# Performance work log

Measured on AMD Instinct MI355X. Metric: run time of the kernel, lower is better.

The kernel has to match this reference:

```python
import jax, jax.numpy as jnp
import numpy as np

D_EMBED = 1024
D_HEAD = 128


def setup_inputs() -> dict:
    key = jax.random.key(0)
    kx, kq, kk, kv = jax.random.split(key, 4)
    x = jax.random.normal(kx, (4, 4096, D_EMBED), dtype=jnp.float32)
    # nn.Linear(d_embed, d_head, bias=False) weights, stored [out, in] like torch
    s = 1.0 / np.sqrt(D_EMBED)
    Wq = jax.random.uniform(kq, (D_HEAD, D_EMBED), jnp.float32, -s, s)
    Wk = jax.random.uniform(kk, (D_HEAD, D_EMBED), jnp.float32, -s, s)
    Wv = jax.random.uniform(kv, (D_HEAD, D_EMBED), jnp.float32, -s, s)
    return {"x": x, "Wq": Wq, "Wk": Wk, "Wv": Wv}


def reference(x, Wq, Wk, Wv):
    # q,k,v: [b, s, d_head]
    q = jnp.einsum("bse,he->bsh", x, Wq)
    k = jnp.einsum("bse,he->bsh", x, Wk)
    v = jnp.einsum("bse,he->bsh", x, Wv)
    # original: (q @ k^T) * d_head**-0.5, then divided by sqrt(d_embed)
    scale = 1.0 / (np.sqrt(D_HEAD) * np.sqrt(D_EMBED))
    scores = jnp.einsum("bqh,bkh->bqk", q, k) * jnp.float32(scale)  # [b, s, s]
    attn = jax.nn.softmax(scores, axis=-1)
    return jnp.einsum("bqk,bkh->bqh", attn, v)
```

## Files before the change

### kernel.cpp

```cpp
#include <hip/hip_runtime.h>
#include <stdint.h>

typedef __bf16 bf16x8 __attribute__((ext_vector_type(8)));
typedef float  f32x4  __attribute__((ext_vector_type(4)));

#define ATTN_SCALE 2.7621359e-3f

__device__ __forceinline__ unsigned short f2bf(float f) {
  union { float f; uint32_t u; } v; v.f = f;
  uint32_t u = v.u;
  uint32_t r = (u + 0x7FFFu + ((u >> 16) & 1u)) >> 16;
  return (unsigned short)r;
}

__device__ __forceinline__ void load_lds16(const unsigned short* g, unsigned short* l) {
  __builtin_amdgcn_global_load_lds(
      (const __attribute__((address_space(1))) void*)g,
      (__attribute__((address_space(3))) void*)l, 16, 0, 0);
}

__device__ __forceinline__ f32x4 mfma16(bf16x8 a, bf16x8 b, f32x4 c) {
  return __builtin_amdgcn_mfma_f32_16x16x32_bf16(a, b, c, 0, 0, 0);
}

__device__ __forceinline__ bf16x8 ones_bf16() {
  union { unsigned short u[8]; bf16x8 v; } c;
#pragma unroll
  for (int j = 0; j < 8; ++j) c.u[j] = 0x3F80;
  return c.v;
}

__global__ __launch_bounds__(256) void k_cvtw(const float* __restrict__ a,
                                              const float* __restrict__ b,
                                              const float* __restrict__ c,
                                              unsigned short* __restrict__ dst) {
  int i = blockIdx.x * 256 + threadIdx.x;
  int sel = i >> 15, off = i & 32767;
  const float* s = (sel == 0) ? a : (sel == 1) ? b : c;
  float4 f = ((const float4*)s)[off];
  ushort4 o;
  o.x = f2bf(f.x); o.y = f2bf(f.y); o.z = f2bf(f.z); o.w = f2bf(f.w);
  ((ushort4*)dst)[i] = o;
}

__global__ __launch_bounds__(256, 3) void k_proj(
    const float* __restrict__ X,
    const unsigned short* __restrict__ W,
    unsigned short* __restrict__ Qb,
    unsigned short* __restrict__ Kb,
    unsigned short* __restrict__ Vt)
{
  __shared__ __align__(16) unsigned short sm[2048 + 4096];
  unsigned short* As = sm;
  unsigned short* Bs = sm + 2048;
  const int t = threadIdx.x;
  const int mtile = blockIdx.x;
  const int nt = blockIdx.y;
  const int w = t >> 6, lane = t & 63, quad = lane >> 4, l15 = lane & 15;
  const int wm = w & 1, wn = w >> 1;

  const float* ag0 = X + (size_t)(mtile * 64 + (t >> 2)) * 1024 + (t & 3) * 8;
  const unsigned short* bg0 = W + (size_t)nt * 131072 + (size_t)(t >> 2) * 1024 + (t & 3) * 8;
  unsigned short* aw = &As[(t >> 2) * 32 + (t & 3) * 8];
  unsigned short* bw = &Bs[(t >> 2) * 32 + (t & 3) * 8];

  f32x4 acc[2][4] = {};

  for (int kt = 0; kt < 32; ++kt) {
    float4 a0 = *(const float4*)(ag0 + kt * 32);
    float4 a1 = *(const float4*)(ag0 + kt * 32 + 4);
    __syncthreads();
    load_lds16(bg0 + kt * 32,             bw);
    load_lds16(bg0 + kt * 32 + 64 * 1024, bw + 2048);
    union { unsigned short u[8]; uint4 v; } pa;
    pa.u[0] = f2bf(a0.x); pa.u[1] = f2bf(a0.y);
    pa.u[2] = f2bf(a0.z); pa.u[3] = f2bf(a0.w);
    pa.u[4] = f2bf(a1.x); pa.u[5] = f2bf(a1.y);
    pa.u[6] = f2bf(a1.z); pa.u[7] = f2bf(a1.w);
    *(uint4*)aw = pa.v;
    __syncthreads();

    bf16x8 af[2], bfr[4];
#pragma unroll
    for (int i = 0; i < 2; ++i)
      af[i] = *(const bf16x8*)&As[(wm * 32 + i * 16 + l15) * 32 + quad * 8];
#pragma unroll
    for (int j = 0; j < 4; ++j)
      bfr[j] = *(const bf16x8*)&Bs[(wn * 64 + j * 16 + l15) * 32 + quad * 8];
#pragma unroll
    for (int i = 0; i < 2; ++i)
#pragma unroll
      for (int j = 0; j < 4; ++j)
        acc[i][j] = mfma16(af[i], bfr[j], acc[i][j]);
  }

  if (nt != 2) {
    const int m0 = mtile * 64 + wm * 32;
#pragma unroll
    for (int i = 0; i < 2; ++i)
#pragma unroll
      for (int j = 0; j < 4; ++j)
#pragma unroll
        for (int r = 0; r < 4; ++r) {
          int m = m0 + i * 16 + quad * 4 + r;
          int n = wn * 64 + j * 16 + l15;
          float v = acc[i][j][r];
          if (nt == 0) Qb[(size_t)m * 128 + n] = f2bf(v * ATTN_SCALE);
          else         Kb[(size_t)m * 128 + n] = f2bf(v);
        }
  } else {
    float* Ts = (float*)sm;
    const int bb = mtile >> 6;
    const int s0 = (mtile & 63) * 64;
#pragma unroll
    for (int jj = 0; jj < 8; ++jj) {
      __syncthreads();
      if (wn == (jj >> 2)) {
        const int j = jj & 3;
#pragma unroll
        for (int i = 0; i < 2; ++i)
#pragma unroll
          for (int r = 0; r < 4; ++r)
            Ts[(wm * 32 + i * 16 + quad * 4 + r) * 17 + l15] = acc[i][j][r];
      }
      __syncthreads();
      int n2 = jj * 16 + (t >> 4);
      int m2 = (t & 15) * 4;
      union { unsigned short u[4]; uint2 v; } pk;
#pragma unroll
      for (int e = 0; e < 4; ++e) pk.u[e] = f2bf(Ts[(m2 + e) * 17 + (t >> 4)]);
      *(uint2*)&Vt[((size_t)(bb * 128 + n2)) * 4096 + s0 + m2] = pk.v;
    }
  }
}

__global__ __launch_bounds__(256, 3) void k_flash(
    const unsigned short* __restrict__ Qb,
    const unsigned short* __restrict__ Kb,
    const unsigned short* __restrict__ Vt,
    float* __restrict__ Om,
    float* __restrict__ lp)
{
  __shared__ __align__(16) unsigned short smem[21504];
  unsigned short* Psh = smem + 16384;
  float* Ob  = (float*)smem;
  float* lsh = (float*)(smem + 16384);

  const int t = threadIdx.x;
  const int w = t >> 6, lane = t & 63, quad = lane >> 4, l15 = lane & 15;
  const int h = w & 1, p = w >> 1;
  const int bid = blockIdx.x;
  const int b   = (bid & 7) >> 1;
  const int sp  = bid & 1;
  const int qt  = bid >> 3;

  const unsigned short* Qg = Qb + (size_t)(b * 4096 + qt * 64 + h * 32) * 128;
  const unsigned short* Kg = Kb + (size_t)b * 4096 * 128;
  const unsigned short* Vg = Vt + (size_t)b * 128 * 4096;

  bf16x8 qf[2][4];
#pragma unroll
  for (int mt = 0; mt < 2; ++mt)
#pragma unroll
    for (int kk = 0; kk < 4; ++kk)
      qf[mt][kk] = *(const bf16x8*)&Qg[(size_t)(mt * 16 + l15) * 128 + kk * 32 + quad * 8];

  f32x4 O[2][8] = {};
  f32x4 Ol[2] = {};

  const unsigned short* kg0 = Kg + (size_t)(t >> 4) * 128 + (((t & 15) ^ ((t >> 5) & 7)) * 8);
  const unsigned short* vg0 = Vg + (size_t)(t >> 3) * 4096 + (((t & 7) ^ ((t >> 3) & 7)) * 8);
  unsigned short* kw = &smem[w * 512];
  unsigned short* vw = &smem[8192 + w * 512];

  const int kt0 = sp * 32;

  {
    const unsigned short* kg = kg0 + (size_t)kt0 * 8192;
#pragma unroll
    for (int it = 0; it < 4; ++it)
      load_lds16(kg + it * 2048, kw + it * 2048);
  }

  for (int i = 0; i < 32; ++i) {
    const int kt = kt0 + i;
    const int ktn = (i < 31) ? (kt + 1) : kt0;

    asm volatile("s_waitcnt vmcnt(0)" ::: "memory");
    asm volatile("s_barrier" ::: "memory");

    {
      const unsigned short* vg = vg0 + (size_t)kt * 64;
#pragma unroll
      for (int it = 0; it < 4; ++it)
        load_lds16(vg + (size_t)it * 131072, vw + it * 2048);
    }

    f32x4 sc[2][2] = {};
#pragma unroll
    for (int ntk = 0; ntk < 2; ++ntk) {
      const int row = p * 32 + 2 * l15 + ntk;
#pragma unroll
      for (int kk = 0; kk < 4; ++kk) {
        bf16x8 kf = *(const bf16x8*)&smem[row * 128 + (((kk * 4 + quad) ^ (l15 & 7)) * 8)];
        sc[0][ntk] = mfma16(qf[0][kk], kf, sc[0][ntk]);
        sc[1][ntk] = mfma16(qf[1][kk], kf, sc[1][ntk]);
      }
    }

#pragma unroll
    for (int mt = 0; mt < 2; ++mt)
#pragma unroll
      for (int r = 0; r < 4; ++r) {
        float e0 = __expf(sc[mt][0][r]);
        float e1 = __expf(sc[mt][1][r]);
        int row = mt * 16 + quad * 4 + r;
        uint32_t pk = (uint32_t)f2bf(e0) | ((uint32_t)f2bf(e1) << 16);
        *(uint32_t*)&Psh[w * 1280 + row * 40 + 2 * l15] = pk;
      }

    asm volatile("s_waitcnt vmcnt(0) lgkmcnt(0)" ::: "memory");
    asm volatile("s_barrier" ::: "memory");

    {
      const unsigned short* kg = kg0 + (size_t)ktn * 8192;
#pragma unroll
      for (int it = 0; it < 4; ++it)
        load_lds16(kg + it * 2048, kw + it * 2048);
    }

    bf16x8 pf0 = *(const bf16x8*)&Psh[w * 1280 + l15 * 40 + quad * 8];
    bf16x8 pf1 = *(const bf16x8*)&Psh[w * 1280 + (16 + l15) * 40 + quad * 8];
    const bf16x8 one = ones_bf16();
    Ol[0] = mfma16(pf0, one, Ol[0]);
    Ol[1] = mfma16(pf1, one, Ol[1]);
    const unsigned short* Vshc = &smem[8192];
#pragma unroll
    for (int dt = 0; dt < 8; ++dt) {
      bf16x8 vf = *(const bf16x8*)&Vshc[(dt * 16 + l15) * 64 + (((p * 4 + quad) ^ (l15 & 7)) * 8)];
      O[0][dt] = mfma16(pf0, vf, O[0][dt]);
      O[1][dt] = mfma16(pf1, vf, O[1][dt]);
    }
  }

  __syncthreads();
  if (p == 1) {
#pragma unroll
    for (int mt = 0; mt < 2; ++mt)
#pragma unroll
      for (int r = 0; r < 4; ++r) {
        int row = h * 32 + mt * 16 + quad * 4 + r;
        if (l15 == 0) lsh[row] = Ol[mt][r];
#pragma unroll
        for (int dt = 0; dt < 8; ++dt)
          Ob[row * 128 + dt * 16 + l15] = O[mt][dt][r];
      }
  }
  __syncthreads();
  if (p == 0) {
    const size_t rowbase = (size_t)b * 4096 + qt * 64;
    float* Omp = Om + (size_t)sp * 2097152;
#pragma unroll
    for (int mt = 0; mt < 2; ++mt)
#pragma unroll
      for (int r = 0; r < 4; ++r) {
        int row = h * 32 + mt * 16 + quad * 4 + r;
#pragma unroll
        for (int dt = 0; dt < 8; ++dt)
          Omp[(rowbase + row) * 128 + dt * 16 + l15] =
              O[mt][dt][r] + Ob[row * 128 + dt * 16 + l15];
        if (l15 == 0)
          lp[(size_t)sp * 16384 + rowbase + row] = Ol[mt][r] + lsh[row];
      }
  }
}

__global__ __launch_bounds__(256) void k_merge(const float* __restrict__ Om,
                                               const float* __restrict__ lp,
                                               float* __restrict__ out) {
  int i = blockIdx.x * 256 + threadIdx.x;
  int row = i >> 5;
  float inv = 1.0f / (lp[row] + lp[16384 + row]);
  float4 a = ((const float4*)Om)[i];
  float4 c = ((const float4*)Om)[524288 + i];
  float4 o;
  o.x = (a.x + c.x) * inv;
  o.y = (a.y + c.y) * inv;
  o.z = (a.z + c.z) * inv;
  o.w = (a.w + c.w) * inv;
  ((float4*)out)[i] = o;
}

extern "C" void kernel_launch(void* const* d_in, const int* in_sizes, int n_in,
                              void* d_out, int out_size, void* d_ws, size_t ws_size,
                              hipStream_t stream) {
  const float* x  = (const float*)d_in[0];
  const float* Wq = (const float*)d_in[1];
  const float* Wk = (const float*)d_in[2];
  const float* Wv = (const float*)d_in[3];
  float* out = (float*)d_out;

  unsigned short* ws  = (unsigned short*)d_ws;
  unsigned short* wbf = ws;
  unsigned short* Qb  = wbf + 393216;
  unsigned short* Kb  = Qb + 2097152;
  unsigned short* Vt  = Kb + 2097152;
  float* Om = (float*)(Vt + 2097152);
  float* lp = Om + 4194304;

  k_cvtw<<<384, 256, 0, stream>>>(Wq, Wk, Wv, wbf);
  k_proj<<<dim3(256, 3), 256, 0, stream>>>(x, wbf, Qb, Kb, Vt);
  k_flash<<<512, 256, 0, stream>>>(Qb, Kb, Vt, Om, lp);
  k_merge<<<2048, 256, 0, stream>>>(Om, lp, out);
}
```

Baseline: 178.5 us.

## Fuse QKV projection into one block per row tile; stagger flash K/V order

The projection kernel now computes Q, K and V together in one block per 64-row tile, each warp covering 96 output columns. X is read and converted to bf16 once instead of three times, and the next X tile is prefetched into registers. The grid drops from 768 to 256 blocks with occupancy 1, which risks lower parallelism and more register pressure. The flash kernel also rotates the starting KV tile per query tile so concurrent blocks read different K/V rows, easing cache and channel contention.

```diff
diff --git a/kernel.cpp b/kernel.cpp
--- a/kernel.cpp
+++ b/kernel.cpp
@@ -43,94 +43,101 @@
   ((ushort4*)dst)[i] = o;
 }
 
-__global__ __launch_bounds__(256, 3) void k_proj(
+__global__ __launch_bounds__(256, 1) void k_proj(
     const float* __restrict__ X,
     const unsigned short* __restrict__ W,
     unsigned short* __restrict__ Qb,
     unsigned short* __restrict__ Kb,
     unsigned short* __restrict__ Vt)
 {
-  __shared__ __align__(16) unsigned short sm[2048 + 4096];
+  __shared__ __align__(16) unsigned short sm[2048 + 12288];
   unsigned short* As = sm;
   unsigned short* Bs = sm + 2048;
   const int t = threadIdx.x;
   const int mtile = blockIdx.x;
-  const int nt = blockIdx.y;
   const int w = t >> 6, lane = t & 63, quad = lane >> 4, l15 = lane & 15;
-  const int wm = w & 1, wn = w >> 1;
 
   const float* ag0 = X + (size_t)(mtile * 64 + (t >> 2)) * 1024 + (t & 3) * 8;
-  const unsigned short* bg0 = W + (size_t)nt * 131072 + (size_t)(t >> 2) * 1024 + (t & 3) * 8;
-  unsigned short* aw = &As[(t >> 2) * 32 + (t & 3) * 8];
-  unsigned short* bw = &Bs[(t >> 2) * 32 + (t & 3) * 8];
-
-  f32x4 acc[2][4] = {};
+  const unsigned short* bg0 = W + (size_t)(t >> 2) * 1024 + (t & 3) * 8;
+  unsigned short* aw = &As[t * 8];
+  unsigned short* bw = &Bs[t * 8];
+
+  f32x4 acc[4][6] = {};
+
+  float4 a0 = *(const float4*)(ag0);
+  float4 a1 = *(const float4*)(ag0 + 4);
 
   for (int kt = 0; kt < 32; ++kt) {
-    float4 a0 = *(const float4*)(ag0 + kt * 32);
-    float4 a1 = *(const float4*)(ag0 + kt * 32 + 4);
     __syncthreads();
-    load_lds16(bg0 + kt * 32,             bw);
-    load_lds16(bg0 + kt * 32 + 64 * 1024, bw + 2048);
+#pragma unroll
+    for (int it = 0; it < 6; ++it)
+      load_lds16(bg0 + kt * 32 + it * 65536, bw + it * 2048);
     union { unsigned short u[8]; uint4 v; } pa;
     pa.u[0] = f2bf(a0.x); pa.u[1] = f2bf(a0.y);
     pa.u[2] = f2bf(a0.z); pa.u[3] = f2bf(a0.w);
     pa.u[4] = f2bf(a1.x); pa.u[5] = f2bf(a1.y);
     pa.u[6] = f2bf(a1.z); pa.u[7] = f2bf(a1.w);
     *(uint4*)aw = pa.v;
+    if (kt < 31) {
+      a0 = *(const float4*)(ag0 + (kt + 1) * 32);
+      a1 = *(const float4*)(ag0 + (kt + 1) * 32 + 4);
+    }
     __syncthreads();
 
-    bf16x8 af[2], bfr[4];
-#pragma unroll
-    for (int i = 0; i < 2; ++i)
-      af[i] = *(const bf16x8*)&As[(wm * 32 + i * 16 + l15) * 32 + quad * 8];
-#pragma unroll
-    for (int j = 0; j < 4; ++j)
-      bfr[j] = *(const bf16x8*)&Bs[(wn * 64 + j * 16 + l15) * 32 + quad * 8];
-#pragma unroll
-    for (int i = 0; i < 2; ++i)
-#pragma unroll
-      for (int j = 0; j < 4; ++j)
+    bf16x8 af[4], bfr[6];
+#pragma unroll
+    for (int i = 0; i < 4; ++i)
+      af[i] = *(const bf16x8*)&As[(i * 16 + l15) * 32 + quad * 8];
+#pragma unroll
+    for (int j = 0; j < 6; ++j)
+      bfr[j] = *(const bf16x8*)&Bs[(w * 96 + j * 16 + l15) * 32 + quad * 8];
+#pragma unroll
+    for (int i = 0; i < 4; ++i)
+#pragma unroll
+      for (int j = 0; j < 6; ++j)
         acc[i][j] = mfma16(af[i], bfr[j], acc[i][j]);
   }
 
-  if (nt != 2) {
-    const int m0 = mtile * 64 + wm * 32;
-#pragma unroll
-    for (int i = 0; i < 2; ++i)
-#pragma unroll
-      for (int j = 0; j < 4; ++j)
+  const int m0 = mtile * 64;
+#pragma unroll
+  for (int j = 0; j < 6; ++j) {
+    const int f = w * 6 + j;
+    if (f < 16) {
+#pragma unroll
+      for (int i = 0; i < 4; ++i)
 #pragma unroll
         for (int r = 0; r < 4; ++r) {
           int m = m0 + i * 16 + quad * 4 + r;
-          int n = wn * 64 + j * 16 + l15;
+          int n = f * 16 + l15;
           float v = acc[i][j][r];
-          if (nt == 0) Qb[(size_t)m * 128 + n] = f2bf(v * ATTN_SCALE);
-          else         Kb[(size_t)m * 128 + n] = f2bf(v);
+          if (f < 8) Qb[(size_t)m * 128 + n]         = f2bf(v * ATTN_SCALE);
+          else       Kb[(size_t)m * 128 + (n - 128)] = f2bf(v);
         }
-  } else {
-    float* Ts = (float*)sm;
-    const int bb = mtile >> 6;
-    const int s0 = (mtile & 63) * 64;
-#pragma unroll
-    for (int jj = 0; jj < 8; ++jj) {
-      __syncthreads();
-      if (wn == (jj >> 2)) {
-        const int j = jj & 3;
-#pragma unroll
-        for (int i = 0; i < 2; ++i)
-#pragma unroll
-          for (int r = 0; r < 4; ++r)
-            Ts[(wm * 32 + i * 16 + quad * 4 + r) * 17 + l15] = acc[i][j][r];
-      }
-      __syncthreads();
-      int n2 = jj * 16 + (t >> 4);
-      int m2 = (t & 15) * 4;
-      union { unsigned short u[4]; uint2 v; } pk;
-#pragma unroll
-      for (int e = 0; e < 4; ++e) pk.u[e] = f2bf(Ts[(m2 + e) * 17 + (t >> 4)]);
-      *(uint2*)&Vt[((size_t)(bb * 128 + n2)) * 4096 + s0 + m2] = pk.v;
-    }
+    }
+  }
+
+  float* Ts = (float*)sm;
+  const int bb = mtile >> 6;
+  const int s0 = (mtile & 63) * 64;
+#pragma unroll
+  for (int c = 0; c < 8; ++c) {
+    const int wv = (c < 2) ? 2 : 3;
+    const int jv = (c < 2) ? (4 + c) : (c - 2);
+    __syncthreads();
+    if (w == wv) {
+#pragma unroll
+      for (int i = 0; i < 4; ++i)
+#pragma unroll
+        for (int r = 0; r < 4; ++r)
+          Ts[(i * 16 + quad * 4 + r) * 17 + l15] = acc[i][jv][r];
+    }
+    __syncthreads();
+    int n2 = c * 16 + (t >> 4);
+    int m2 = (t & 15) * 4;
+    union { unsigned short u[4]; uint2 v; } pk;
+#pragma unroll
+    for (int e = 0; e < 4; ++e) pk.u[e] = f2bf(Ts[(m2 + e) * 17 + (t >> 4)]);
+    *(uint2*)&Vt[((size_t)(bb * 128 + n2)) * 4096 + s0 + m2] = pk.v;
   }
 }
 
@@ -174,17 +181,18 @@
   unsigned short* vw = &smem[8192 + w * 512];
 
   const int kt0 = sp * 32;
+  const int off = (qt & 3) * 8;
 
   {
-    const unsigned short* kg = kg0 + (size_t)kt0 * 8192;
+    const unsigned short* kg = kg0 + (size_t)(kt0 + off) * 8192;
 #pragma unroll
     for (int it = 0; it < 4; ++it)
       load_lds16(kg + it * 2048, kw + it * 2048);
   }
 
   for (int i = 0; i < 32; ++i) {
-    const int kt = kt0 + i;
-    const int ktn = (i < 31) ? (kt + 1) : kt0;
+    const int kt  = kt0 + ((i + off) & 31);
+    const int ktn = kt0 + ((i + 1 + off) & 31);
 
     asm volatile("s_waitcnt vmcnt(0)" ::: "memory");
     asm volatile("s_barrier" ::: "memory");
@@ -309,7 +317,7 @@
   float* lp = Om + 4194304;
 
   k_cvtw<<<384, 256, 0, stream>>>(Wq, Wk, Wv, wbf);
-  k_proj<<<dim3(256, 3), 256, 0, stream>>>(x, wbf, Qb, Kb, Vt);
+  k_proj<<<256, 256, 0, stream>>>(x, wbf, Qb, Kb, Vt);
   k_flash<<<512, 256, 0, stream>>>(Qb, Kb, Vt, Om, lp);
   k_merge<<<2048, 256, 0, stream>>>(Om, lp, out);
 }
```

After: 193.0 us. 8.1% more time.

## Fuse weight bf16 conversion into projection kernel and prefetch next K tile

Applied to the files above, without the earlier changes.

Drops the separate weight-conversion kernel launch. The projection kernel now reads fp32 weights directly, converts them to bf16 in registers and writes them to LDS. It also register-prefetches the next k-tile of X and W while the current tile is being computed. This removes one launch and the intermediate weight buffer round-trip. In exchange each projection block redundantly converts weights, reads twice the weight bytes, and uses more registers.

```diff
diff --git a/kernel.cpp b/kernel.cpp
--- a/kernel.cpp
+++ b/kernel.cpp
@@ -30,22 +30,11 @@
   return c.v;
 }
 
-__global__ __launch_bounds__(256) void k_cvtw(const float* __restrict__ a,
-                                              const float* __restrict__ b,
-                                              const float* __restrict__ c,
-                                              unsigned short* __restrict__ dst) {
-  int i = blockIdx.x * 256 + threadIdx.x;
-  int sel = i >> 15, off = i & 32767;
-  const float* s = (sel == 0) ? a : (sel == 1) ? b : c;
-  float4 f = ((const float4*)s)[off];
-  ushort4 o;
-  o.x = f2bf(f.x); o.y = f2bf(f.y); o.z = f2bf(f.z); o.w = f2bf(f.w);
-  ((ushort4*)dst)[i] = o;
-}
-
 __global__ __launch_bounds__(256, 3) void k_proj(
     const float* __restrict__ X,
-    const unsigned short* __restrict__ W,
+    const float* __restrict__ Wq,
+    const float* __restrict__ Wk,
+    const float* __restrict__ Wv,
     unsigned short* __restrict__ Qb,
     unsigned short* __restrict__ Kb,
     unsigned short* __restrict__ Vt)
@@ -59,25 +48,51 @@
   const int w = t >> 6, lane = t & 63, quad = lane >> 4, l15 = lane & 15;
   const int wm = w & 1, wn = w >> 1;
 
+  const float* Wsel = (nt == 0) ? Wq : (nt == 1) ? Wk : Wv;
+
   const float* ag0 = X + (size_t)(mtile * 64 + (t >> 2)) * 1024 + (t & 3) * 8;
-  const unsigned short* bg0 = W + (size_t)nt * 131072 + (size_t)(t >> 2) * 1024 + (t & 3) * 8;
-  unsigned short* aw = &As[(t >> 2) * 32 + (t & 3) * 8];
-  unsigned short* bw = &Bs[(t >> 2) * 32 + (t & 3) * 8];
+  const float* bg0 = Wsel + (size_t)(t >> 2) * 1024 + (t & 3) * 8;
+  unsigned short* aw = &As[t * 8];
+  unsigned short* bw = &Bs[t * 8];
 
   f32x4 acc[2][4] = {};
 
+  float4 a0 = *(const float4*)(ag0);
+  float4 a1 = *(const float4*)(ag0 + 4);
+  float4 b0 = *(const float4*)(bg0);
+  float4 b1 = *(const float4*)(bg0 + 4);
+  float4 b2 = *(const float4*)(bg0 + 65536);
+  float4 b3 = *(const float4*)(bg0 + 65536 + 4);
+
   for (int kt = 0; kt < 32; ++kt) {
-    float4 a0 = *(const float4*)(ag0 + kt * 32);
-    float4 a1 = *(const float4*)(ag0 + kt * 32 + 4);
     __syncthreads();
-    load_lds16(bg0 + kt * 32,             bw);
-    load_lds16(bg0 + kt * 32 + 64 * 1024, bw + 2048);
-    union { unsigned short u[8]; uint4 v; } pa;
-    pa.u[0] = f2bf(a0.x); pa.u[1] = f2bf(a0.y);
-    pa.u[2] = f2bf(a0.z); pa.u[3] = f2bf(a0.w);
-    pa.u[4] = f2bf(a1.x); pa.u[5] = f2bf(a1.y);
-    pa.u[6] = f2bf(a1.z); pa.u[7] = f2bf(a1.w);
-    *(uint4*)aw = pa.v;
+    {
+      union { unsigned short u[8]; uint4 v; } pa;
+      pa.u[0] = f2bf(a0.x); pa.u[1] = f2bf(a0.y);
+      pa.u[2] = f2bf(a0.z); pa.u[3] = f2bf(a0.w);
+      pa.u[4] = f2bf(a1.x); pa.u[5] = f2bf(a1.y);
+      pa.u[6] = f2bf(a1.z); pa.u[7] = f2bf(a1.w);
+      *(uint4*)aw = pa.v;
+      union { unsigned short u[8]; uint4 v; } pb;
+      pb.u[0] = f2bf(b0.x); pb.u[1] = f2bf(b0.y);
+      pb.u[2] = f2bf(b0.z); pb.u[3] = f2bf(b0.w);
+      pb.u[4] = f2bf(b1.x); pb.u[5] = f2bf(b1.y);
+      pb.u[6] = f2bf(b1.z); pb.u[7] = f2bf(b1.w);
+      *(uint4*)bw = pb.v;
+      pb.u[0] = f2bf(b2.x); pb.u[1] = f2bf(b2.y);
+      pb.u[2] = f2bf(b2.z); pb.u[3] = f2bf(b2.w);
+      pb.u[4] = f2bf(b3.x); pb.u[5] = f2bf(b3.y);
+      pb.u[6] = f2bf(b3.z); pb.u[7] = f2bf(b3.w);
+      *(uint4*)(bw + 2048) = pb.v;
+    }
+    if (kt < 31) {
+      a0 = *(const float4*)(ag0 + (kt + 1) * 32);
+      a1 = *(const float4*)(ag0 + (kt + 1) * 32 + 4);
+      b0 = *(const float4*)(bg0 + (kt + 1) * 32);
+      b1 = *(const float4*)(bg0 + (kt + 1) * 32 + 4);
+      b2 = *(const float4*)(bg0 + (kt + 1) * 32 + 65536);
+      b3 = *(const float4*)(bg0 + (kt + 1) * 32 + 65536 + 4);
+    }
     __syncthreads();
 
     bf16x8 af[2], bfr[4];
@@ -301,15 +316,13 @@
   float* out = (float*)d_out;
 
   unsigned short* ws  = (unsigned short*)d_ws;
-  unsigned short* wbf = ws;
-  unsigned short* Qb  = wbf + 393216;
+  unsigned short* Qb  = ws;
   unsigned short* Kb  = Qb + 2097152;
   unsigned short* Vt  = Kb + 2097152;
   float* Om = (float*)(Vt + 2097152);
   float* lp = Om + 4194304;
 
-  k_cvtw<<<384, 256, 0, stream>>>(Wq, Wk, Wv, wbf);
-  k_proj<<<dim3(256, 3), 256, 0, stream>>>(x, wbf, Qb, Kb, Vt);
+  k_proj<<<dim3(256, 3), 256, 0, stream>>>(x, Wq, Wk, Wv, Qb, Kb, Vt);
   k_flash<<<512, 256, 0, stream>>>(Qb, Kb, Vt, Om, lp);
   k_merge<<<2048, 256, 0, stream>>>(Om, lp, out);
 }
```

After: 179.6 us. Within noise of the previous version (+0.6%).

## Double-buffer W tiles and prefetch X registers in projection GEMM loop

Applied to the files above, without the earlier changes.

Restructures the projection GEMM main loop into a software pipeline. The next K-tile of W is loaded asynchronously into a second LDS buffer and the next X values are prefetched into registers while the current tile is converted and multiplied. Raw s_waitcnt/s_barrier asm replaces __syncthreads so the prefetch loads can stay in flight across the barrier. This doubles the B-tile LDS footprint, which may lower occupancy, and relies on hand-counted vmcnt values being correct.

```diff
diff --git a/kernel.cpp b/kernel.cpp
--- a/kernel.cpp
+++ b/kernel.cpp
@@ -50,7 +50,7 @@
     unsigned short* __restrict__ Kb,
     unsigned short* __restrict__ Vt)
 {
-  __shared__ __align__(16) unsigned short sm[2048 + 4096];
+  __shared__ __align__(16) unsigned short sm[2048 + 8192];
   unsigned short* As = sm;
   unsigned short* Bs = sm + 2048;
   const int t = threadIdx.x;
@@ -61,37 +61,61 @@
 
   const float* ag0 = X + (size_t)(mtile * 64 + (t >> 2)) * 1024 + (t & 3) * 8;
   const unsigned short* bg0 = W + (size_t)nt * 131072 + (size_t)(t >> 2) * 1024 + (t & 3) * 8;
-  unsigned short* aw = &As[(t >> 2) * 32 + (t & 3) * 8];
-  unsigned short* bw = &Bs[(t >> 2) * 32 + (t & 3) * 8];
+  unsigned short* aw  = &As[t * 8];
+  unsigned short* bw0 = &Bs[t * 8];
+  unsigned short* bw1 = &Bs[4096 + t * 8];
 
   f32x4 acc[2][4] = {};
 
+  load_lds16(bg0,             bw0);
+  load_lds16(bg0 + 64 * 1024, bw0 + 2048);
+  float4 a0 = *(const float4*)(ag0);
+  float4 a1 = *(const float4*)(ag0 + 4);
+
   for (int kt = 0; kt < 32; ++kt) {
-    float4 a0 = *(const float4*)(ag0 + kt * 32);
-    float4 a1 = *(const float4*)(ag0 + kt * 32 + 4);
-    __syncthreads();
-    load_lds16(bg0 + kt * 32,             bw);
-    load_lds16(bg0 + kt * 32 + 64 * 1024, bw + 2048);
-    union { unsigned short u[8]; uint4 v; } pa;
-    pa.u[0] = f2bf(a0.x); pa.u[1] = f2bf(a0.y);
-    pa.u[2] = f2bf(a0.z); pa.u[3] = f2bf(a0.w);
-    pa.u[4] = f2bf(a1.x); pa.u[5] = f2bf(a1.y);
-    pa.u[6] = f2bf(a1.z); pa.u[7] = f2bf(a1.w);
-    *(uint4*)aw = pa.v;
-    __syncthreads();
-
+    const int cur = kt & 1, nxt = cur ^ 1;
+
+    asm volatile("s_waitcnt lgkmcnt(0)" ::: "memory");
+    asm volatile("s_barrier" ::: "memory");
+
+    unsigned short* bwn = nxt ? bw1 : bw0;
+    if (kt < 31) {
+      load_lds16(bg0 + (kt + 1) * 32,             bwn);
+      load_lds16(bg0 + (kt + 1) * 32 + 64 * 1024, bwn + 2048);
+    }
+    float4 na0 = a0, na1 = a1;
+    if (kt < 31) {
+      na0 = *(const float4*)(ag0 + (kt + 1) * 32);
+      na1 = *(const float4*)(ag0 + (kt + 1) * 32 + 4);
+    }
+
+    {
+      union { unsigned short u[8]; uint4 v; } pa;
+      pa.u[0] = f2bf(a0.x); pa.u[1] = f2bf(a0.y);
+      pa.u[2] = f2bf(a0.z); pa.u[3] = f2bf(a0.w);
+      pa.u[4] = f2bf(a1.x); pa.u[5] = f2bf(a1.y);
+      pa.u[6] = f2bf(a1.z); pa.u[7] = f2bf(a1.w);
+      *(uint4*)aw = pa.v;
+    }
+
+    asm volatile("s_waitcnt vmcnt(4) lgkmcnt(0)" ::: "memory");
+    asm volatile("s_barrier" ::: "memory");
+
+    const unsigned short* Bc = Bs + cur * 4096;
     bf16x8 af[2], bfr[4];
 #pragma unroll
     for (int i = 0; i < 2; ++i)
       af[i] = *(const bf16x8*)&As[(wm * 32 + i * 16 + l15) * 32 + quad * 8];
 #pragma unroll
     for (int j = 0; j < 4; ++j)
-      bfr[j] = *(const bf16x8*)&Bs[(wn * 64 + j * 16 + l15) * 32 + quad * 8];
+      bfr[j] = *(const bf16x8*)&Bc[(wn * 64 + j * 16 + l15) * 32 + quad * 8];
 #pragma unroll
     for (int i = 0; i < 2; ++i)
 #pragma unroll
       for (int j = 0; j < 4; ++j)
         acc[i][j] = mfma16(af[i], bfr[j], acc[i][j]);
+
+    a0 = na0; a1 = na1;
   }
 
   if (nt != 2) {
```

New measurement: 185.4 us. 3.8% more time.
